# Optimization experiments

Measured on AMD Instinct MI355X. Metric: run time of the kernel, lower is better.

The kernel has to match this reference:

```python
import jax, jax.numpy as jnp
import numpy as np

B, T_ENC, T_DEC = 64, 512, 800
N_MEL, ENC_DIM = 80, 512
ATTN_RNN, DEC_RNN, PRENET, ATTN_DIM = 1024, 1024, 256, 128
N_FILT, KSIZE = 32, 31
PAD = (KSIZE - 1) // 2


def _lstm_cell(x, h, c, Wi, Wh, bi, bh):
    # torch.nn.LSTMCell gate order: i, f, g, o
    g = x @ Wi.T + bi + h @ Wh.T + bh
    i, f, gg, o = jnp.split(g, 4, axis=-1)
    c2 = jax.nn.sigmoid(f) * c + jax.nn.sigmoid(i) * jnp.tanh(gg)
    h2 = jax.nn.sigmoid(o) * jnp.tanh(c2)
    return h2, c2


def setup_inputs() -> dict:
    key = jax.random.key(0)
    ks = iter(jax.random.split(key, 32))

    def rn(shape, s=0.02):
        return jax.random.normal(next(ks), shape, jnp.float32) * s

    return dict(
        memory=jax.random.normal(next(ks), (B, T_ENC, ENC_DIM), jnp.float32),
        decoder_inputs=jax.random.normal(next(ks), (T_DEC, B, N_MEL), jnp.float32),
        memory_lengths=jax.random.randint(next(ks), (B,), T_ENC // 2, T_ENC + 1, jnp.int32),
        W1=rn((PRENET, N_MEL)), b1=jnp.zeros((PRENET,), jnp.float32),
        W2=rn((PRENET, PRENET)), b2=jnp.zeros((PRENET,), jnp.float32),
        Wi_a=rn((4 * ATTN_RNN, PRENET + ENC_DIM)), Wh_a=rn((4 * ATTN_RNN, ATTN_RNN)),
        bi_a=jnp.zeros((4 * ATTN_RNN,), jnp.float32), bh_a=jnp.zeros((4 * ATTN_RNN,), jnp.float32),
        Wq=rn((ATTN_DIM, ATTN_RNN)), Wm=rn((ATTN_DIM, ENC_DIM)), v=rn((ATTN_DIM,)),
        Wloc=rn((N_FILT, 2, KSIZE)), Wld=rn((ATTN_DIM, N_FILT)),
        Wi_d=rn((4 * DEC_RNN, ATTN_RNN + ENC_DIM)), Wh_d=rn((4 * DEC_RNN, DEC_RNN)),
        bi_d=jnp.zeros((4 * DEC_RNN,), jnp.float32), bh_d=jnp.zeros((4 * DEC_RNN,), jnp.float32),
        Wp=rn((N_MEL, DEC_RNN + ENC_DIM)), bp=jnp.zeros((N_MEL,), jnp.float32),
        Wg=rn((1, DEC_RNN + ENC_DIM)), bg=jnp.zeros((1,), jnp.float32),
    )


def reference(memory, decoder_inputs, memory_lengths,
              W1, b1, W2, b2,
              Wi_a, Wh_a, bi_a, bh_a,
              Wq, Wm, v, Wloc, Wld,
              Wi_d, Wh_d, bi_d, bh_d,
              Wp, bp, Wg, bg):
    # go frame + teacher-forced inputs, prenet applied to all steps at once
    go = jnp.zeros((1, B, N_MEL), memory.dtype)
    di = jnp.concatenate([go, decoder_inputs], axis=0)[:T_DEC]        # [Td,B,80]
    x = jax.nn.relu(di @ W1.T + b1)
    x = jax.nn.relu(x @ W2.T + b2)                                    # [Td,B,256] (prenet dropout p=0)

    pmem = memory @ Wm.T                                              # [B,T,128] processed memory
    pad_mask = jnp.arange(T_ENC)[None, :] >= memory_lengths[:, None]  # True = padding

    def step(carry, xt):
        ah, ac, dh, dc, aw, awc, ctx = carry
        # attention RNN
        ah, ac = _lstm_cell(jnp.concatenate([xt, ctx], -1), ah, ac, Wi_a, Wh_a, bi_a, bh_a)
        # location-sensitive attention
        cat = jnp.stack([aw, awc], axis=1)                            # [B,2,T]
        loc = jax.lax.conv_general_dilated(cat, Wloc, (1,), [(PAD, PAD)],
                                           dimension_numbers=('NCH', 'OIH', 'NCH'))  # [B,32,T]
        loc = jnp.einsum('bft,df->btd', loc, Wld)                     # [B,T,128]
        pq = (ah @ Wq.T)[:, None, :]                                  # [B,1,128]
        e = jnp.tanh(pq + loc + pmem) @ v                             # [B,T]
        e = jnp.where(pad_mask, -jnp.inf, e)
        aw_new = jax.nn.softmax(e, axis=1)
        ctx_new = jnp.einsum('bt,btd->bd', aw_new, memory)            # [B,512]
        awc_new = awc + aw_new
        # decoder RNN + projections
        dh, dc = _lstm_cell(jnp.concatenate([ah, ctx_new], -1), dh, dc, Wi_d, Wh_d, bi_d, bh_d)
        hc = jnp.concatenate([dh, ctx_new], -1)                       # [B,1536]
        mel = hc @ Wp.T + bp                                          # [B,80]
        gate = (hc @ Wg.T + bg)[:, 0]                                 # [B]
        return (ah, ac, dh, dc, aw_new, awc_new, ctx_new), (mel, gate, aw_new)

    z = lambda d: jnp.zeros((B, d), memory.dtype)
    carry0 = (z(ATTN_RNN), z(ATTN_RNN), z(DEC_RNN), z(DEC_RNN),
              z(T_ENC), z(T_ENC), z(ENC_DIM))
    _, (mels, gates, aws) = jax.lax.scan(step, carry0, x)

    mel_outputs = jnp.transpose(mels, (1, 0, 2)).reshape(B, -1, N_MEL)  # [B,Td,80]
    gate_outputs = jnp.transpose(gates, (1, 0))                          # [B,Td]
    alignments = jnp.transpose(aws, (1, 0, 2))                           # [B,Td,T]
    return mel_outputs, gate_outputs, alignments
```

## Files before the change

kernel.cpp:

```cpp
#include <hip/hip_runtime.h>
#include <stdint.h>

#define TDEC 800
#define NBATCH 64
#define TE 512
#define ED 512
#define NMEL 80
#define PRE 256
#define AR 1024
#define AD 128

typedef unsigned short u16;
typedef __bf16 bf16x8 __attribute__((ext_vector_type(8)));
typedef float f32x4 __attribute__((ext_vector_type(4)));

struct Args {
  const float *mem, *dec_in; const int *mlen;
  const float *W1, *b1, *W2, *b2;
  const float *Wi_a, *Wh_a, *bi_a, *bh_a;
  const float *Wq, *Wm, *v_in, *Wloc, *Wld;
  const float *Wi_d, *Wh_d, *bi_d, *bh_d;
  const float *Wp, *bp, *Wg, *bg;
  int *grp_cnt, *root_cnt, *gen_root, *gen_grp, *pq_flag, *done_pad;
  float *expsum_pad;
  u16 *ab, *db, *hctx;
  float *aw, *awc, *exp_e, *pq;
  u16 *x_all, *pmem_bf, *mem_bf, *hid_bf;
  u16 *WaSwz, *WdSwz, *WqSwz, *WpgSwz, *U2Swz;
  float *bias_a, *bias_d, *bpg;
  float *out_mel, *out_gate, *out_align;
};

__device__ __forceinline__ float b2f(u16 h){ return __uint_as_float(((uint32_t)h) << 16); }
__device__ __forceinline__ u16 f2b(float f){
  uint32_t u = __float_as_uint(f);
  uint32_t r = (u + 0x7fffu + ((u >> 16) & 1u)) >> 16;
  return (u16)r;
}
__device__ __forceinline__ float sigm(float x){ return 1.f / (1.f + __expf(-x)); }
__device__ __forceinline__ float tanh_(float x){ float e = __expf(2.f*x); return 1.f - 2.f/(e + 1.f); }

__device__ __forceinline__ f32x4 mfma16(bf16x8 a, bf16x8 b, f32x4 c){
  return __builtin_amdgcn_mfma_f32_16x16x32_bf16(a, b, c, 0, 0, 0);
}
__device__ __forceinline__ bf16x8 ldf(const u16* p){ return *(const bf16x8*)p; }

__device__ __forceinline__ unsigned long long ald64(const void* p){
  return __hip_atomic_load((const unsigned long long*)p, __ATOMIC_RELAXED, __HIP_MEMORY_SCOPE_AGENT);
}
__device__ __forceinline__ void ast64(void* p, unsigned long long v){
  __hip_atomic_store((unsigned long long*)p, v, __ATOMIC_RELAXED, __HIP_MEMORY_SCOPE_AGENT);
}
__device__ __forceinline__ float aldf(const float* p){
  return __hip_atomic_load(p, __ATOMIC_RELAXED, __HIP_MEMORY_SCOPE_AGENT);
}
__device__ __forceinline__ void astf(float* p, float v){
  __hip_atomic_store(p, v, __ATOMIC_RELAXED, __HIP_MEMORY_SCOPE_AGENT);
}
__device__ __forceinline__ void asti(int* p, int v){
  __hip_atomic_store(p, v, __ATOMIC_RELAXED, __HIP_MEMORY_SCOPE_AGENT);
}
__device__ __forceinline__ bf16x8 ldbm(const u16* baseP, int c0, int row){
  const u16* p = baseP + (((size_t)(c0 >> 2)) << 8) + (row << 2);
  union { unsigned long long u[2]; bf16x8 v; } r;
  r.u[0] = ald64(p); r.u[1] = ald64(p + 256);
  return r.v;
}
__device__ __forceinline__ bf16x8 ldct(const u16* p){
  union { unsigned long long u[2]; bf16x8 v; } r;
  r.u[0] = ald64(p); r.u[1] = ald64(p + 4);
  return r.v;
}

__device__ void gbar(const Args& A, int blk, int tid, int bt){
  __syncthreads();
  if (tid == 0){
    int g = blk >> 5;
    int old = __hip_atomic_fetch_add(&A.grp_cnt[g*16], 1, __ATOMIC_RELAXED, __HIP_MEMORY_SCOPE_AGENT);
    if (old == bt*32 - 1){
      int ro = __hip_atomic_fetch_add(&A.root_cnt[0], 1, __ATOMIC_RELAXED, __HIP_MEMORY_SCOPE_AGENT);
      if (ro == bt*8 - 1){
        __hip_atomic_store(&A.gen_root[0], bt, __ATOMIC_RELAXED, __HIP_MEMORY_SCOPE_AGENT);
      } else {
        while (__hip_atomic_load(&A.gen_root[0], __ATOMIC_RELAXED, __HIP_MEMORY_SCOPE_AGENT) < bt)
          __builtin_amdgcn_s_sleep(2);
      }
      __hip_atomic_store(&A.gen_grp[g*16], bt, __ATOMIC_RELAXED, __HIP_MEMORY_SCOPE_AGENT);
    } else {
      while (__hip_atomic_load(&A.gen_grp[g*16], __ATOMIC_RELAXED, __HIP_MEMORY_SCOPE_AGENT) < bt)
        __builtin_amdgcn_s_sleep(4);
    }
  }
  __syncthreads();
}

template<bool DO_A>
__device__ __forceinline__ void gemmF(const Args& A, int t, int tid,
                                      const u16* sWa, const u16* sWd,
                                      float* sGa, float* sGd){
  const int pc = t & 1, pp = (t + 1) & 1;
  const int wave = tid >> 6, lane = tid & 63;
  const int row = wave*16 + (lane & 15);
  const int kg = (lane >> 4) << 3;
  const u16* abP  = A.ab + (size_t)pp * 65536;
  const u16* dbP  = A.db + (size_t)pc * 65536;
  const u16* ctxP = A.hctx + (size_t)pp * NBATCH * 512 + (size_t)row * 512;
  const u16* x0   = A.x_all + ((size_t)t * NBATCH + row) * PRE;

  f32x4 aA0 = {0.f,0.f,0.f,0.f}, aA1 = aA0, aD0 = aA0, aD1 = aA0;

  if (DO_A){
    bf16x8 fx[8];
    #pragma unroll
    for (int j = 0; j < 8; ++j) fx[j] = ldf(x0 + j*32 + kg);
    #pragma unroll
    for (int j = 0; j < 8; ++j){
      bf16x8 w = *(const bf16x8*)(sWa + ((size_t)j*64 + lane)*8);
      if (j & 1) aA1 = mfma16(fx[j], w, aA1); else aA0 = mfma16(fx[j], w, aA0);
    }
  }
  auto ldfrag = [&](int kk) -> bf16x8 {
    if (kk < 32)      return ldbm(abP, kk*32 + kg, row);
    else if (kk < 48) return ldct(ctxP + (kk - 32)*32 + kg);
    else              return ldbm(dbP, (kk - 48)*32 + kg, row);
  };
  bf16x8 fA[16], fB[16];
  #pragma unroll
  for (int j = 0; j < 16; ++j) fA[j] = ldfrag(j);
  #pragma unroll
  for (int B = 0; B < 5; ++B){
    const bf16x8* cur = (B & 1) ? fB : fA;
    bf16x8*       nxt = (B & 1) ? fA : fB;
    if (B < 4){
      #pragma unroll
      for (int j = 0; j < 16; ++j) nxt[j] = ldfrag((B + 1)*16 + j);
    }
    #pragma unroll
    for (int j = 0; j < 16; ++j){
      const int kk = B*16 + j;
      bf16x8 f = cur[j];
      bf16x8 wd = *(const bf16x8*)(sWd + ((size_t)kk*64 + lane)*8);
      if (kk & 1) aD1 = mfma16(f, wd, aD1); else aD0 = mfma16(f, wd, aD0);
      if (DO_A && kk < 48){
        const int ka = (kk < 32) ? (24 + kk) : (kk - 24);
        bf16x8 wa = *(const bf16x8*)(sWa + ((size_t)ka*64 + lane)*8);
        if (kk & 1) aA1 = mfma16(f, wa, aA1); else aA0 = mfma16(f, wa, aA0);
      }
    }
  }
  const int r0 = wave*16 + ((lane >> 4) << 2), col = lane & 15;
  f32x4 aD = aD0 + aD1;
  #pragma unroll
  for (int r = 0; r < 4; ++r) sGd[(r0 + r)*17 + col] = aD[r];
  if (DO_A){
    f32x4 aA = aA0 + aA1;
    #pragma unroll
    for (int r = 0; r < 4; ++r) sGa[(r0 + r)*17 + col] = aA[r];
  }
}

__device__ __forceinline__ void pwise(int tid, const float* sG, const float* b4,
                                      float& cst, u16* sH){
  int bb = tid & 63, ci = tid >> 6;
  int j4 = ci * 4;
  float gi = sG[bb*17 + j4 + 0] + b4[0];
  float gf = sG[bb*17 + j4 + 1] + b4[1];
  float gg = sG[bb*17 + j4 + 2] + b4[2];
  float go = sG[bb*17 + j4 + 3] + b4[3];
  float cn = sigm(gf) * cst + sigm(gi) * tanh_(gg);
  cst = cn;
  sH[bb*4 + ci] = f2b(sigm(go) * tanh_(cn));
}

__device__ __forceinline__ void loc_chunk(int tl0, int tid, u16* sLoc,
                                          const float* s_awh, const float* s_awch,
                                          const bf16x8* U2reg){
  int wave = tid >> 6, lane = tid & 63;
  int tg0 = tl0 + wave*16 + (lane & 15);
  int kk0 = (lane >> 4) << 3;
  f32x4 acc[8];
  #pragma unroll
  for (int nt = 0; nt < 8; ++nt) acc[nt] = f32x4{0.f,0.f,0.f,0.f};
  #pragma unroll
  for (int kt = 0; kt < 2; ++kt){
    const float* src = kt ? s_awch : s_awh;
    int base = tg0 - 15 + kk0;
    union { u16 h[8]; bf16x8 v; } af;
    #pragma unroll
    for (int j = 0; j < 8; ++j) af.h[j] = f2b(src[base + j]);
    #pragma unroll
    for (int nt = 0; nt < 8; ++nt) acc[nt] = mfma16(af.v, U2reg[kt*8 + nt], acc[nt]);
  }
  int rrow = wave*16 + ((lane>>4)<<2);
  #pragma unroll
  for (int nt = 0; nt < 8; ++nt){
    int d = nt*16 + (lane & 15);
    #pragma unroll
    for (int r = 0; r < 4; ++r) sLoc[(rrow + r)*132 + d] = f2b(acc[nt][r]);
  }
}

__device__ __forceinline__ float e_chunk(const Args& A, int b, int tb, int tid,
                                         const u16* sLoc, const float* s_pq,
                                         const float* s_v, int mlen){
  int tl = tid >> 2, h4 = tid & 3;
  int tg = tb + tl;
  int d0 = h4 * 32;
  const u16* prow = A.pmem_bf + ((size_t)b*TE + tg)*AD + d0;
  const u16* lrow = sLoc + tl*132 + d0;
  float s = 0.f;
  #pragma unroll
  for (int dq = 0; dq < 4; ++dq){
    bf16x8 pv = ldf(prow + dq*8);
    bf16x8 lv = *(const bf16x8*)(lrow + dq*8);
    #pragma unroll
    for (int j = 0; j < 8; ++j){
      int d = d0 + dq*8 + j;
      float arg = s_pq[d] + (float)lv[j] + (float)pv[j];
      s += tanh_(arg) * s_v[d];
    }
  }
  s += __shfl_xor(s, 1); s += __shfl_xor(s, 2);
  float ex = 0.f;
  if (h4 == 0 && tg < mlen) ex = __expf(s);
  if (h4 == 0) astf(&A.exp_e[(size_t)b*TE + tg], ex);
  return ex;
}

__device__ __forceinline__ void ctx_unit(const Args& A, int t, int b, int c, int tid,
                                         float inv, const float* s_exp, float* s_ctx,
                                         u16* sH16, int mlen){
  int wave = tid >> 6, lane = tid & 63;
  int dseg = lane & 15, rr = lane >> 4;
  const u16* mb = A.mem_bf + ((size_t)b*TE)*ED + c*128 + dseg*8;
  float a[8] = {0.f,0.f,0.f,0.f,0.f,0.f,0.f,0.f};
  int tbase = wave * 128;
  int rem = mlen - tbase;
  int icnt = rem <= 0 ? 0 : ((rem + 3) >> 2);
  if (icnt > 32) icnt = 32;
  #pragma unroll 8
  for (int i = 0; i < icnt; ++i){
    int tt = tbase + i*4 + rr;
    float wt = s_exp[tt];
    bf16x8 mv = ldf(mb + (size_t)tt * ED);
    #pragma unroll
    for (int j = 0; j < 8; ++j) a[j] += wt * (float)mv[j];
  }
  #pragma unroll
  for (int j = 0; j < 8; ++j){ a[j] += __shfl_xor(a[j], 16); a[j] += __shfl_xor(a[j], 32); }
  if (lane < 16){
    #pragma unroll
    for (int j = 0; j < 8; ++j) s_ctx[wave*128 + dseg*8 + j] = a[j];
  }
  __syncthreads();
  if (tid < 128)
    sH16[tid] = f2b((s_ctx[tid] + s_ctx[128+tid] + s_ctx[256+tid] + s_ctx[384+tid]) * inv);
  __syncthreads();
  if (tid < 32)
    ast64(A.hctx + (size_t)(t&1)*NBATCH*512 + (size_t)b*512 + c*128 + tid*4,
          *(const unsigned long long*)(sH16 + tid*4));
}

__device__ __forceinline__ void pq_unit(const Args& A, int t, int s, int tid){
  int pc = t & 1;
  int wave = tid >> 6, lane = tid & 63;
  int m = wave*16 + (lane & 15), kg = (lane >> 4) << 3;
  const u16* abP = A.ab + (size_t)pc * 65536;
  f32x4 acc = {0.f,0.f,0.f,0.f};
  #pragma unroll 8
  for (int kt = 0; kt < 32; ++kt){
    bf16x8 af = ldbm(abP, kt*32 + kg, m);
    bf16x8 bb = ldf(A.WqSwz + (((size_t)s*32 + kt)*64 + lane)*8);
    acc = mfma16(af, bb, acc);
  }
  int r0 = wave*16 + ((lane>>4)<<2);
  int d = s*16 + (lane & 15);
  #pragma unroll
  for (int r = 0; r < 4; ++r) astf(&A.pq[(size_t)(r0+r)*AD + d], acc[r]);
}

__device__ __forceinline__ void proj_unit(const Args& A, int t, int ns, int tid){
  const int pp = (t + 1) & 1;
  int wave = tid >> 6, lane = tid & 63;
  int m = wave*16 + (lane & 15), kg = (lane >> 4) << 3;
  const u16* dbP = A.db + (size_t)pp * 65536;
  const u16* cxP = A.hctx + (size_t)pp * NBATCH * 512 + (size_t)m * 512;
  int n = ns*16 + (lane & 15);
  float bv = A.bpg[n];
  f32x4 acc = {bv, bv, bv, bv};
  #pragma unroll 8
  for (int kt = 0; kt < 48; ++kt){
    bf16x8 af = (kt < 32) ? ldbm(dbP, kt*32 + kg, m) : ldct(cxP + kt*32 + kg - 1024);
    bf16x8 bb = ldf(A.WpgSwz + (((size_t)ns*48 + kt)*64 + lane)*8);
    acc = mfma16(af, bb, acc);
  }
  int r0 = wave*16 + ((lane>>4)<<2);
  #pragma unroll
  for (int r = 0; r < 4; ++r){
    int bb2 = r0 + r;
    if (n < 80)       A.out_mel[((size_t)bb2*TDEC + (t-1))*NMEL + n] = acc[r];
    else if (n == 80) A.out_gate[(size_t)bb2*TDEC + (t-1)] = acc[r];
  }
}

__global__ __launch_bounds__(256, 1) void k_main(Args A){
  __shared__ u16 sWa[28672];
  __shared__ u16 sWd[40960];
  __shared__ __align__(16) char sBuf[16896];
  __shared__ float s_pq[128], s_v[128], s_ctx[512], s_red[4];
  __shared__ float s_exp[512];
  __shared__ float s_awh[160], s_awch[160];
  __shared__ u16 sH16[128];
  float* sGa = (float*)sBuf;
  float* sGd = (float*)(sBuf + 4352);
  u16*   sHa = (u16*)(sBuf + 8704);
  u16*   sHd = (u16*)(sBuf + 9216);
  u16*   sLoc = (u16*)sBuf;
  const int bn = blockIdx.x, tid = threadIdx.x;
  const int c = bn >> 6, b = bn & 63;
  {
    const uint4* ga = (const uint4*)(A.WaSwz + (size_t)bn*28672);
    for (int i = tid; i < 3584; i += 256) ((uint4*)sWa)[i] = ga[i];
    const uint4* gd = (const uint4*)(A.WdSwz + (size_t)bn*40960);
    for (int i = tid; i < 5120; i += 256) ((uint4*)sWd)[i] = gd[i];
  }
  if (tid < 128) s_v[tid] = A.v_in[tid];
  bf16x8 U2reg[16];
  #pragma unroll
  for (int kt = 0; kt < 2; ++kt)
    #pragma unroll
    for (int nt = 0; nt < 8; ++nt)
      U2reg[kt*8 + nt] = ldf(A.U2Swz + ((size_t)((nt*2 + kt)*64 + (tid & 63)))*8);
  float ba4[4], bd4[4];
  {
    int cb = bn*16 + (tid >> 6)*4;
    #pragma unroll
    for (int g = 0; g < 4; ++g){ ba4[g] = A.bias_a[cb+g]; bd4[g] = A.bias_d[cb+g]; }
  }
  float c_a = 0.f, c_d = 0.f;
  float awc_reg0 = 0.f, awc_reg1 = 0.f;
  const int mlen = A.mlen[b];
  __syncthreads();
  int bt = 0;
  #pragma unroll 1
  for (int t = 0; t <= TDEC; ++t){
    if (t < TDEC) gemmF<true >(A, t, tid, sWa, sWd, sGa, sGd);
    else          gemmF<false>(A, t, tid, sWa, sWd, sGa, sGd);
    __syncthreads();
    if (t < TDEC) pwise(tid, sGa, ba4, c_a, sHa);
    if (t >= 1)   pwise(tid, sGd, bd4, c_d, sHd);
    __syncthreads();
    if (tid < 64){
      if (t < TDEC)
        ast64(A.ab + (size_t)(t&1)*65536 + (size_t)bn*256 + tid*4,
              *(const unsigned long long*)(sHa + tid*4));
    } else if (tid < 128){
      if (t >= 1)
        ast64(A.db + (size_t)((t+1)&1)*65536 + (size_t)bn*256 + (size_t)(tid-64)*4,
              *(const unsigned long long*)(sHd + (tid-64)*4));
    }
    if (t < TDEC && bn == 255){
      if (tid >= 128 && tid < 192) astf(&A.expsum_pad[(tid-128)*16], 0.f);
      else if (tid >= 192)         asti(&A.done_pad[(tid-192)*16], 0);
      if (tid == 128)              asti(&A.pq_flag[0], 0);
    }
    gbar(A, bn, tid, ++bt);
    if (t < TDEC){
      if (bn >= 64 && bn < 72){
        pq_unit(A, t, bn - 64, tid);
        __syncthreads();
        if (tid == 0)
          __hip_atomic_fetch_add(&A.pq_flag[0], 1, __ATOMIC_RELAXED, __HIP_MEMORY_SCOPE_AGENT);
      }
      if (t >= 1 && bn >= 72 && bn < 78) proj_unit(A, t, bn - 72, tid);
      const int tb = c * 128;
      const bool w0 = tb < mlen, w1 = (tb + 64) < mlen;
      if (w0){
        for (int i = tid; i < 160; i += 256){
          int idx = tb - 15 + i;
          bool v = (idx >= 0 && idx < TE);
          s_awh[i]  = v ? aldf(&A.aw[(size_t)b*TE + idx]) : 0.f;
          s_awch[i] = v ? aldf(&A.awc[(size_t)b*TE + idx]) : 0.f;
        }
      }
      __syncthreads();
      float ws = 0.f;
      if (w0) loc_chunk(15, tid, sLoc, s_awh, s_awch, U2reg);
      __syncthreads();
      if (tid == 0){
        while (__hip_atomic_load(&A.pq_flag[0], __ATOMIC_RELAXED, __HIP_MEMORY_SCOPE_AGENT) < 8)
          __builtin_amdgcn_s_sleep(8);
      }
      __syncthreads();
      if (tid < 128) s_pq[tid] = aldf(&A.pq[(size_t)b*AD + tid]);
      __syncthreads();
      if (w0) ws = e_chunk(A, b, tb, tid, sLoc, s_pq, s_v, mlen);
      __syncthreads();
      if (w1){
        loc_chunk(79, tid, sLoc, s_awh, s_awch, U2reg);
        __syncthreads();
        ws += e_chunk(A, b, tb + 64, tid, sLoc, s_pq, s_v, mlen);
      }
      #pragma unroll
      for (int o = 32; o >= 1; o >>= 1) ws += __shfl_xor(ws, o);
      if ((tid & 63) == 0) s_red[tid >> 6] = ws;
      __syncthreads();
      if (tid == 0){
        float tot = s_red[0] + s_red[1] + s_red[2] + s_red[3];
        __hip_atomic_fetch_add(&A.expsum_pad[b*16], tot, __ATOMIC_RELAXED, __HIP_MEMORY_SCOPE_AGENT);
        asm volatile("s_waitcnt vmcnt(0)" ::: "memory");
        __hip_atomic_fetch_add(&A.done_pad[b*16], 1, __ATOMIC_RELAXED, __HIP_MEMORY_SCOPE_AGENT);
        while (__hip_atomic_load(&A.done_pad[b*16], __ATOMIC_RELAXED, __HIP_MEMORY_SCOPE_AGENT) < 4)
          __builtin_amdgcn_s_sleep(4);
      }
      __syncthreads();
      float inv = 1.f / aldf(&A.expsum_pad[b*16]);
      {
        unsigned long long u = ald64(&A.exp_e[(size_t)b*TE + tid*2]);
        s_exp[tid*2]     = __uint_as_float((uint32_t)u);
        s_exp[tid*2 + 1] = __uint_as_float((uint32_t)(u >> 32));
      }
      __syncthreads();
      ctx_unit(A, t, b, c, tid, inv, s_exp, s_ctx, sH16, mlen);
      if (c == 0){
        float awt0 = s_exp[tid] * inv;
        float awt1 = s_exp[tid + 256] * inv;
        astf(&A.aw[(size_t)b*TE + tid], awt0);
        astf(&A.aw[(size_t)b*TE + tid + 256], awt1);
        awc_reg0 += awt0; awc_reg1 += awt1;
        astf(&A.awc[(size_t)b*TE + tid], awc_reg0);
        astf(&A.awc[(size_t)b*TE + tid + 256], awc_reg1);
        A.out_align[((size_t)b*TDEC + t)*TE + tid] = awt0;
        A.out_align[((size_t)b*TDEC + t)*TE + tid + 256] = awt1;
      }
      gbar(A, bn, tid, ++bt);
    } else {
      if (bn >= 72 && bn < 78) proj_unit(A, t, bn - 72, tid);
    }
  }
}

__global__ void k_prenet1(Args A){
  __shared__ float din[8 * 80];
  int g0 = blockIdx.x * 8;
  for (int idx = threadIdx.x; idx < 640; idx += 256){
    int r = idx / 80, k = idx % 80;
    int row = g0 + r;
    int t = row >> 6, b = row & 63;
    din[idx] = (t == 0) ? 0.f : A.dec_in[((size_t)(t - 1) * NBATCH + b) * NMEL + k];
  }
  __syncthreads();
  int j = threadIdx.x;
  float acc[8] = {0,0,0,0,0,0,0,0};
  for (int k = 0; k < 80; ++k){
    float w = A.W1[(size_t)j * 80 + k];
    #pragma unroll
    for (int r = 0; r < 8; ++r) acc[r] += w * din[r * 80 + k];
  }
  float bb = A.b1[j];
  #pragma unroll
  for (int r = 0; r < 8; ++r){
    float vx = acc[r] + bb; if (vx < 0.f) vx = 0.f;
    A.hid_bf[(size_t)(g0 + r) * PRE + j] = f2b(vx);
  }
}

__global__ void k_prenet2(Args A){
  __shared__ float hrow[8 * 256];
  int g0 = blockIdx.x * 8;
  for (int idx = threadIdx.x; idx < 2048; idx += 256){
    int r = idx >> 8, k = idx & 255;
    hrow[idx] = b2f(A.hid_bf[(size_t)(g0 + r) * PRE + k]);
  }
  __syncthreads();
  int j = threadIdx.x;
  float acc[8] = {0,0,0,0,0,0,0,0};
  for (int k = 0; k < 256; ++k){
    float w = A.W2[(size_t)j * PRE + k];
    #pragma unroll
    for (int r = 0; r < 8; ++r) acc[r] += w * hrow[r * 256 + k];
  }
  float bb = A.b2[j];
  #pragma unroll
  for (int r = 0; r < 8; ++r){
    float vx = acc[r] + bb; if (vx < 0.f) vx = 0.f;
    A.x_all[(size_t)(g0 + r) * PRE + j] = f2b(vx);
  }
}

__global__ void k_membf(Args A){
  size_t n = (size_t)NBATCH * TE * ED;
  for (size_t i = (size_t)blockIdx.x * 256 + threadIdx.x; i < n; i += (size_t)gridDim.x * 256)
    A.mem_bf[i] = f2b(A.mem[i]);
}

__global__ void k_pmem(Args A){
  __shared__ float mrow[8 * 512];
  int g0 = blockIdx.x * 8;
  for (int idx = threadIdx.x; idx < 4096; idx += 256){
    int r = idx >> 9, k = idx & 511;
    mrow[idx] = A.mem[(size_t)(g0 + r) * ED + k];
  }
  __syncthreads();
  int d = threadIdx.x & 127, hh = threadIdx.x >> 7;
  float acc[4] = {0,0,0,0};
  for (int k = 0; k < 512; ++k){
    float w = A.Wm[(size_t)d * ED + k];
    #pragma unroll
    for (int r = 0; r < 4; ++r) acc[r] += w * mrow[(hh * 4 + r) * 512 + k];
  }
  #pragma unroll
  for (int r = 0; r < 4; ++r)
    A.pmem_bf[(size_t)(g0 + hh * 4 + r) * AD + d] = f2b(acc[r]);
}

__global__ void k_swz(Args A){
  const size_t Na = 917504, Nd = 1310720, Nq = 16384, Npg = 18432, Nu2 = 1024;
  const size_t NT = Na + Nd + Nq + Npg + Nu2;
  size_t id = (size_t)blockIdx.x * 256 + threadIdx.x;
  if (id >= NT + 8288) return;
  if (id < NT){
    int which; size_t lid; int NKT; u16* dst;
    if (id < Na){ which = 0; lid = id; NKT = 56; dst = A.WaSwz; }
    else if (id < Na + Nd){ which = 1; lid = id - Na; NKT = 80; dst = A.WdSwz; }
    else if (id < Na + Nd + Nq){ which = 2; lid = id - Na - Nd; NKT = 32; dst = A.WqSwz; }
    else if (id < Na + Nd + Nq + Npg){ which = 3; lid = id - Na - Nd - Nq; NKT = 48; dst = A.WpgSwz; }
    else { which = 4; lid = id - Na - Nd - Nq - Npg; NKT = 2; dst = A.U2Swz; }
    int lane = lid & 63;
    size_t rem = lid >> 6;
    int kt = (int)(rem % NKT), nt = (int)(rem / NKT);
    int n = (nt << 4) + (lane & 15);
    int k0 = (kt << 5) + ((lane >> 4) << 3);
    union { u16 h[8]; uint4 u; } o;
    #pragma unroll
    for (int j = 0; j < 8; ++j){
      int k = k0 + j;
      float vv = 0.f;
      if (which == 0){
        int rr = (n & 3) * 1024 + (n >> 2);
        vv = (k < 768) ? A.Wi_a[(size_t)rr * 768 + k] : A.Wh_a[(size_t)rr * 1024 + (k - 768)];
      } else if (which == 1){
        int rr = (n & 3) * 1024 + (n >> 2);
        vv = (k < 1536) ? A.Wi_d[(size_t)rr * 1536 + k] : A.Wh_d[(size_t)rr * 1024 + (k - 1536)];
      } else if (which == 2){
        vv = A.Wq[(size_t)n * 1024 + k];
      } else if (which == 3){
        vv = (n < 80) ? A.Wp[(size_t)n * 1536 + k] : ((n == 80) ? A.Wg[k] : 0.f);
      } else {
        int cc = k >> 5, kk = k & 31;
        if (kk < 31){
          float s = 0.f;
          for (int f = 0; f < 32; ++f)
            s += A.Wld[(size_t)n * 32 + f] * A.Wloc[(size_t)(f * 2 + cc) * 31 + kk];
          vv = s;
        }
      }
      o.h[j] = f2b(vv);
    }
    *(uint4*)(dst + lid * 8) = o.u;
  } else {
    size_t bid = id - NT;
    if (bid < 4096){
      int rr = ((int)bid & 3) * 1024 + ((int)bid >> 2);
      A.bias_a[bid] = A.bi_a[rr] + A.bh_a[rr];
    } else if (bid < 8192){
      int n = (int)bid - 4096;
      int rr = (n & 3) * 1024 + (n >> 2);
      A.bias_d[n] = A.bi_d[rr] + A.bh_d[rr];
    } else {
      int n = (int)bid - 8192;
      A.bpg[n] = (n < 80) ? A.bp[n] : ((n == 80) ? A.bg[0] : 0.f);
    }
  }
}

extern "C" void kernel_launch(void* const* d_in, const int* in_sizes, int n_in,
                              void* d_out, int out_size, void* d_ws, size_t ws_size,
                              hipStream_t stream){
  Args A;
  A.mem   = (const float*)d_in[0];
  A.dec_in= (const float*)d_in[1];
  A.mlen  = (const int*)d_in[2];
  A.W1 = (const float*)d_in[3];  A.b1 = (const float*)d_in[4];
  A.W2 = (const float*)d_in[5];  A.b2 = (const float*)d_in[6];
  A.Wi_a = (const float*)d_in[7];  A.Wh_a = (const float*)d_in[8];
  A.bi_a = (const float*)d_in[9];  A.bh_a = (const float*)d_in[10];
  A.Wq = (const float*)d_in[11]; A.Wm = (const float*)d_in[12];
  A.v_in = (const float*)d_in[13];
  A.Wloc = (const float*)d_in[14]; A.Wld = (const float*)d_in[15];
  A.Wi_d = (const float*)d_in[16]; A.Wh_d = (const float*)d_in[17];
  A.bi_d = (const float*)d_in[18]; A.bh_d = (const float*)d_in[19];
  A.Wp = (const float*)d_in[20]; A.bp = (const float*)d_in[21];
  A.Wg = (const float*)d_in[22]; A.bg = (const float*)d_in[23];

  uint8_t* w = (uint8_t*)d_ws;
  size_t cur = 0;
  auto AL = [&](size_t bytes) -> uint8_t* {
    uint8_t* p = w + cur;
    cur = (cur + bytes + 255) & ~(size_t)255;
    return p;
  };
  A.grp_cnt  = (int*)AL(8 * 16 * 4);
  A.root_cnt = (int*)AL(16 * 4);
  A.gen_root = (int*)AL(16 * 4);
  A.gen_grp  = (int*)AL(8 * 16 * 4);
  A.pq_flag  = (int*)AL(16 * 4);
  A.done_pad = (int*)AL(64 * 16 * 4);
  A.expsum_pad = (float*)AL(64 * 16 * 4);
  A.ab   = (u16*)AL((size_t)2 * 65536 * 2);
  A.db   = (u16*)AL((size_t)2 * 65536 * 2);
  A.hctx = (u16*)AL((size_t)2 * 64 * 512 * 2);
  A.aw   = (float*)AL((size_t)64 * 512 * 4);
  A.awc  = (float*)AL((size_t)64 * 512 * 4);
  A.exp_e= (float*)AL((size_t)64 * 512 * 4);
  size_t zbytes = cur;
  A.pq      = (float*)AL((size_t)64 * 128 * 4);
  A.x_all   = (u16*)AL((size_t)TDEC * 64 * 256 * 2);
  A.pmem_bf = (u16*)AL((size_t)64 * 512 * 128 * 2);
  A.WaSwz  = (u16*)AL((size_t)1792 * 4096 * 2);
  A.WdSwz  = (u16*)AL((size_t)2560 * 4096 * 2);
  A.WqSwz  = (u16*)AL((size_t)1024 * 128 * 2);
  A.WpgSwz = (u16*)AL((size_t)1536 * 96 * 2);
  A.U2Swz  = (u16*)AL((size_t)64 * 128 * 2);
  A.bias_a = (float*)AL(4096 * 4);
  A.bias_d = (float*)AL(4096 * 4);
  A.bpg    = (float*)AL(96 * 4);
  A.mem_bf = (u16*)AL((size_t)64 * 512 * 512 * 2);
  A.hid_bf = A.mem_bf;

  float* out = (float*)d_out;
  A.out_mel  = out;
  A.out_gate = out + (size_t)64 * 800 * 80;
  A.out_align= A.out_gate + (size_t)64 * 800;

  hipMemsetAsync(d_ws, 0, zbytes, stream);
  k_prenet1<<<dim3(6400), dim3(256), 0, stream>>>(A);
  k_prenet2<<<dim3(6400), dim3(256), 0, stream>>>(A);
  k_membf<<<dim3(4096), dim3(256), 0, stream>>>(A);
  k_pmem<<<dim3(4096), dim3(256), 0, stream>>>(A);
  k_swz<<<dim3(8877), dim3(256), 0, stream>>>(A);
  k_main<<<dim3(256), dim3(256), 0, stream>>>(A);
}
```

Before: 43.34 ms.

## Switch hidden-state buffers to row-major and use 16-byte sc1 loads with pipelined waits

Changes the global layout of the attention and decoder hidden-state buffers from a column-blocked layout to row-major, so each lane's 8-element fragment is contiguous. Those fragments are then fetched with single 16-byte global loads carrying the sc1 cache bit through inline asm, replacing pairs of 8-byte atomic loads. The GEMM now issues the next batch of loads before waiting on the current one with explicit vmcnt counters, to overlap memory latency with MFMA work. The pq and exp_e reads also become 16-byte loads. The writers now scatter 8-byte stores across rows, and the hand-placed waitcnt instructions must stay correct and keep cross-block data coherent.

```diff
diff --git a/kernel.cpp b/kernel.cpp
--- a/kernel.cpp
+++ b/kernel.cpp
@@ -60,16 +60,19 @@
 __device__ __forceinline__ void asti(int* p, int v){
   __hip_atomic_store(p, v, __ATOMIC_RELAXED, __HIP_MEMORY_SCOPE_AGENT);
 }
-__device__ __forceinline__ bf16x8 ldbm(const u16* baseP, int c0, int row){
-  const u16* p = baseP + (((size_t)(c0 >> 2)) << 8) + (row << 2);
-  union { unsigned long long u[2]; bf16x8 v; } r;
-  r.u[0] = ald64(p); r.u[1] = ald64(p + 256);
-  return r.v;
-}
 __device__ __forceinline__ bf16x8 ldct(const u16* p){
   union { unsigned long long u[2]; bf16x8 v; } r;
   r.u[0] = ald64(p); r.u[1] = ald64(p + 4);
   return r.v;
+}
+__device__ __forceinline__ void issue16(bf16x8& r, const u16* p){
+  asm volatile("global_load_dwordx4 %0, %1, off sc1" : "=v"(r) : "v"(p));
+}
+__device__ __forceinline__ f32x4 ld16f(const float* p){
+  f32x4 r;
+  asm volatile("global_load_dwordx4 %0, %1, off sc1\n\ts_waitcnt vmcnt(0)"
+               : "=v"(r) : "v"(p) : "memory");
+  return r;
 }
 
 __device__ void gbar(const Args& A, int blk, int tid, int bt){
@@ -102,39 +105,44 @@
   const int wave = tid >> 6, lane = tid & 63;
   const int row = wave*16 + (lane & 15);
   const int kg = (lane >> 4) << 3;
-  const u16* abP  = A.ab + (size_t)pp * 65536;
-  const u16* dbP  = A.db + (size_t)pc * 65536;
-  const u16* ctxP = A.hctx + (size_t)pp * NBATCH * 512 + (size_t)row * 512;
-  const u16* x0   = A.x_all + ((size_t)t * NBATCH + row) * PRE;
+  const u16* abP = A.ab + (size_t)pp*65536 + (size_t)row*1024 + kg;
+  const u16* dbP = A.db + (size_t)pc*65536 + (size_t)row*1024 + kg;
+  const u16* cxP = A.hctx + (size_t)pp*32768 + (size_t)row*512 + kg;
+  const u16* x0  = A.x_all + ((size_t)t*NBATCH + row)*PRE + kg;
 
   f32x4 aA0 = {0.f,0.f,0.f,0.f}, aA1 = aA0, aD0 = aA0, aD1 = aA0;
 
   if (DO_A){
     bf16x8 fx[8];
     #pragma unroll
-    for (int j = 0; j < 8; ++j) fx[j] = ldf(x0 + j*32 + kg);
+    for (int j = 0; j < 8; ++j) fx[j] = ldf(x0 + j*32);
     #pragma unroll
     for (int j = 0; j < 8; ++j){
       bf16x8 w = *(const bf16x8*)(sWa + ((size_t)j*64 + lane)*8);
       if (j & 1) aA1 = mfma16(fx[j], w, aA1); else aA0 = mfma16(fx[j], w, aA0);
     }
   }
-  auto ldfrag = [&](int kk) -> bf16x8 {
-    if (kk < 32)      return ldbm(abP, kk*32 + kg, row);
-    else if (kk < 48) return ldct(ctxP + (kk - 32)*32 + kg);
-    else              return ldbm(dbP, (kk - 48)*32 + kg, row);
+  auto addr = [&](int kk) -> const u16* {
+    return (kk < 32) ? (abP + kk*32)
+         : (kk < 48) ? (cxP + (kk - 32)*32)
+         :             (dbP + (kk - 48)*32);
   };
+  asm volatile("s_waitcnt vmcnt(0)" ::: "memory");
   bf16x8 fA[16], fB[16];
   #pragma unroll
-  for (int j = 0; j < 16; ++j) fA[j] = ldfrag(j);
+  for (int j = 0; j < 16; ++j) issue16(fA[j], addr(j));
   #pragma unroll
   for (int B = 0; B < 5; ++B){
+    if (B < 4){
+      bf16x8* nxt = (B & 1) ? fA : fB;
+      #pragma unroll
+      for (int j = 0; j < 16; ++j) issue16(nxt[j], addr((B + 1)*16 + j));
+      asm volatile("s_waitcnt vmcnt(16)" ::: "memory");
+    } else {
+      asm volatile("s_waitcnt vmcnt(0)" ::: "memory");
+    }
+    __builtin_amdgcn_sched_barrier(0);
     const bf16x8* cur = (B & 1) ? fB : fA;
-    bf16x8*       nxt = (B & 1) ? fA : fB;
-    if (B < 4){
-      #pragma unroll
-      for (int j = 0; j < 16; ++j) nxt[j] = ldfrag((B + 1)*16 + j);
-    }
     #pragma unroll
     for (int j = 0; j < 16; ++j){
       const int kk = B*16 + j;
@@ -257,7 +265,7 @@
     sH16[tid] = f2b((s_ctx[tid] + s_ctx[128+tid] + s_ctx[256+tid] + s_ctx[384+tid]) * inv);
   __syncthreads();
   if (tid < 32)
-    ast64(A.hctx + (size_t)(t&1)*NBATCH*512 + (size_t)b*512 + c*128 + tid*4,
+    ast64(A.hctx + (size_t)(t&1)*32768 + (size_t)b*512 + c*128 + tid*4,
           *(const unsigned long long*)(sH16 + tid*4));
 }
 
@@ -265,11 +273,11 @@
   int pc = t & 1;
   int wave = tid >> 6, lane = tid & 63;
   int m = wave*16 + (lane & 15), kg = (lane >> 4) << 3;
-  const u16* abP = A.ab + (size_t)pc * 65536;
+  const u16* ap = A.ab + (size_t)pc*65536 + (size_t)m*1024 + kg;
   f32x4 acc = {0.f,0.f,0.f,0.f};
   #pragma unroll 8
   for (int kt = 0; kt < 32; ++kt){
-    bf16x8 af = ldbm(abP, kt*32 + kg, m);
+    bf16x8 af = ldct(ap + kt*32);
     bf16x8 bb = ldf(A.WqSwz + (((size_t)s*32 + kt)*64 + lane)*8);
     acc = mfma16(af, bb, acc);
   }
@@ -283,14 +291,14 @@
   const int pp = (t + 1) & 1;
   int wave = tid >> 6, lane = tid & 63;
   int m = wave*16 + (lane & 15), kg = (lane >> 4) << 3;
-  const u16* dbP = A.db + (size_t)pp * 65536;
-  const u16* cxP = A.hctx + (size_t)pp * NBATCH * 512 + (size_t)m * 512;
+  const u16* dp = A.db + (size_t)pp*65536 + (size_t)m*1024 + kg;
+  const u16* cp = A.hctx + (size_t)pp*32768 + (size_t)m*512 + kg;
   int n = ns*16 + (lane & 15);
   float bv = A.bpg[n];
   f32x4 acc = {bv, bv, bv, bv};
   #pragma unroll 8
   for (int kt = 0; kt < 48; ++kt){
-    bf16x8 af = (kt < 32) ? ldbm(dbP, kt*32 + kg, m) : ldct(cxP + kt*32 + kg - 1024);
+    bf16x8 af = (kt < 32) ? ldct(dp + kt*32) : ldct(cp + (kt - 32)*32);
     bf16x8 bb = ldf(A.WpgSwz + (((size_t)ns*48 + kt)*64 + lane)*8);
     acc = mfma16(af, bb, acc);
   }
@@ -352,11 +360,11 @@
     __syncthreads();
     if (tid < 64){
       if (t < TDEC)
-        ast64(A.ab + (size_t)(t&1)*65536 + (size_t)bn*256 + tid*4,
+        ast64(A.ab + (size_t)(t&1)*65536 + (size_t)tid*1024 + bn*4,
               *(const unsigned long long*)(sHa + tid*4));
     } else if (tid < 128){
       if (t >= 1)
-        ast64(A.db + (size_t)((t+1)&1)*65536 + (size_t)bn*256 + (size_t)(tid-64)*4,
+        ast64(A.db + (size_t)((t+1)&1)*65536 + (size_t)(tid-64)*1024 + bn*4,
               *(const unsigned long long*)(sHd + (tid-64)*4));
     }
     if (t < TDEC && bn == 255){
@@ -392,7 +400,8 @@
           __builtin_amdgcn_s_sleep(8);
       }
       __syncthreads();
-      if (tid < 128) s_pq[tid] = aldf(&A.pq[(size_t)b*AD + tid]);
+      if (tid < 32)
+        *(f32x4*)&s_pq[tid*4] = ld16f(&A.pq[(size_t)b*AD + tid*4]);
       __syncthreads();
       if (w0) ws = e_chunk(A, b, tb, tid, sLoc, s_pq, s_v, mlen);
       __syncthreads();
@@ -415,11 +424,8 @@
       }
       __syncthreads();
       float inv = 1.f / aldf(&A.expsum_pad[b*16]);
-      {
-        unsigned long long u = ald64(&A.exp_e[(size_t)b*TE + tid*2]);
-        s_exp[tid*2]     = __uint_as_float((uint32_t)u);
-        s_exp[tid*2 + 1] = __uint_as_float((uint32_t)(u >> 32));
-      }
+      if (tid < 128)
+        *(f32x4*)&s_exp[tid*4] = ld16f(&A.exp_e[(size_t)b*TE + tid*4]);
       __syncthreads();
       ctx_unit(A, t, b, c, tid, inv, s_exp, s_ctx, sH16, mlen);
       if (c == 0){
```

Result: faster. 42.34 ms (-2.3%).
